# Kernel tuning notes

Hardware: AMD Instinct MI355X
Metric: run time of the kernel (lower is better)

Reference implementation:

```python
import math
import jax, jax.numpy as jnp
import numpy as np

HEADS = 8


def setup_inputs() -> dict:
    key = jax.random.key(0)
    k1, k2, k3 = jax.random.split(key, 3)
    b, n, a, dim = 1, 256, 256, 512
    init_scale = 0.02
    x = jax.random.normal(k1, (b, n, a, dim), dtype=jnp.float32)
    w_qkv = jax.random.normal(k2, (dim, 3 * dim), dtype=jnp.float32) * init_scale
    b_qkv = jnp.zeros((3 * dim,), dtype=jnp.float32)
    w_proj = jax.random.normal(k3, (dim, dim), dtype=jnp.float32) * init_scale
    b_proj = jnp.zeros((dim,), dtype=jnp.float32)
    return {"x": x, "w_qkv": w_qkv, "b_qkv": b_qkv, "w_proj": w_proj, "b_proj": b_proj}


def reference(x, w_qkv, b_qkv, w_proj, b_proj):
    b, n, a, dim = x.shape
    dh = dim // HEADS
    scale = 1.0 / math.sqrt(math.sqrt(dh))
    qkv = jnp.einsum('bnad,de->bnae', x, w_qkv) + b_qkv  # [b,n,a,3*dim]
    qkv = qkv.reshape(b, n, a, HEADS, 3 * dh)
    q, k, v = jnp.split(qkv, 3, axis=-1)  # each [b,n,a,h,dh]
    # scores over the 'a' axis, independent per (b, n, head)
    sim = jnp.einsum('bnihd,bnjhd->bnhij', q * scale, k * scale)
    attn = jax.nn.softmax(sim, axis=-1)
    out = jnp.einsum('bnhij,bnjhd->bnihd', attn, v).reshape(b, n, a, dim)
    return jnp.einsum('bnad,de->bnae', out, w_proj) + b_proj
```

## Files before the change

### kernel.cpp

```cpp
#include <hip/hip_runtime.h>

typedef unsigned short u16;
typedef unsigned int u32;
typedef __bf16 bf16x8 __attribute__((ext_vector_type(8)));
typedef float f32x4 __attribute__((ext_vector_type(4)));

__device__ __forceinline__ u16 f2b(float f) {
  u32 u = __builtin_bit_cast(u32, f);
  u32 r = (u + 0x7fffu + ((u >> 16) & 1u)) >> 16;
  return (u16)r;
}
__device__ __forceinline__ bf16x8 ld_frag(const u16* p) {
  uint4 v = *(const uint4*)p;
  return __builtin_bit_cast(bf16x8, v);
}
__device__ __forceinline__ void async_lds16(const u16* g, u16* lds) {
  __builtin_amdgcn_global_load_lds(
      (const __attribute__((address_space(1))) void*)g,
      (__attribute__((address_space(3))) void*)lds, 16, 0, 0);
}
__device__ __forceinline__ void wait_lds() { __builtin_amdgcn_s_waitcnt(0xc07f); }

__global__ __launch_bounds__(256) void convert_f32_bf16(const float* __restrict__ in,
                                                        u16* __restrict__ out) {
  long i = ((long)blockIdx.x * 256 + threadIdx.x) * 8;
  float4 a = *(const float4*)(in + i);
  float4 b = *(const float4*)(in + i + 4);
  union { uint4 v; u16 e[8]; } u;
  u.e[0] = f2b(a.x); u.e[1] = f2b(a.y); u.e[2] = f2b(a.z); u.e[3] = f2b(a.w);
  u.e[4] = f2b(b.x); u.e[5] = f2b(b.y); u.e[6] = f2b(b.z); u.e[7] = f2b(b.w);
  *(uint4*)(out + i) = u.v;
}

__global__ __launch_bounds__(256) void transpose_w(const float* __restrict__ W,
                                                   u16* __restrict__ Wt,
                                                   int K, int N) {
  __shared__ alignas(16) u16 T[64][80];
  const int n0 = blockIdx.x * 64, k0 = blockIdx.y * 64;
  const int t = threadIdx.x;
  {
    int kk = t >> 3, c = t & 7;
#pragma unroll
    for (int rr = 0; rr < 2; ++rr) {
      int kr = kk + rr * 32;
      const float* src = W + (long)(k0 + kr) * N + n0 + c * 8;
      float4 a = *(const float4*)src;
      float4 b = *(const float4*)(src + 4);
      u16* dst = &T[kr][c * 8];
      dst[0] = f2b(a.x); dst[1] = f2b(a.y); dst[2] = f2b(a.z); dst[3] = f2b(a.w);
      dst[4] = f2b(b.x); dst[5] = f2b(b.y); dst[6] = f2b(b.z); dst[7] = f2b(b.w);
    }
  }
  __syncthreads();
  {
    int nn = t >> 3, kc = t & 7;
#pragma unroll
    for (int rr = 0; rr < 2; ++rr) {
      int nr = nn + rr * 32;
      union { uint4 v; u16 e[8]; } u;
#pragma unroll
      for (int i = 0; i < 8; ++i) u.e[i] = T[kc * 8 + i][nr];
      *(uint4*)(Wt + (long)(n0 + nr) * K + k0 + kc * 8) = u.v;
    }
  }
}

template <bool OUT_F32>
__global__ __launch_bounds__(256) void gemm_bt(const u16* __restrict__ A,
                                               const u16* __restrict__ Bt,
                                               const float* __restrict__ bias,
                                               void* __restrict__ Cv,
                                               int M, int N, int K) {
  __shared__ alignas(16) u16 As[128 * 32];
  __shared__ alignas(16) u16 Bs[128 * 32];
  const int tid = threadIdx.x;
  const int lane = tid & 63, wave = tid >> 6;
  const int quad = lane >> 4, ln = lane & 15;
  const int wm = wave & 1, wn = wave >> 1;
  const long m0 = (long)blockIdx.y * 128;
  const long n0 = (long)blockIdx.x * 128;

  f32x4 zero = {0.f, 0.f, 0.f, 0.f};
  f32x4 acc[4][4];
#pragma unroll
  for (int i = 0; i < 4; ++i)
#pragma unroll
    for (int j = 0; j < 4; ++j) acc[i][j] = zero;

  const int c1 = tid + 256;
  const int rowA0 = tid >> 2, colA0 = (tid & 3) * 8;
  const int rowA1 = c1 >> 2, colA1 = (c1 & 3) * 8;
  u16* ldsA0 = &As[wave * 512];
  u16* ldsA1 = &As[2048 + wave * 512];
  u16* ldsB0 = &Bs[wave * 512];
  u16* ldsB1 = &Bs[2048 + wave * 512];

  for (int k0 = 0; k0 < K; k0 += 32) {
    async_lds16(A + (m0 + rowA0) * K + k0 + colA0, ldsA0);
    async_lds16(A + (m0 + rowA1) * K + k0 + colA1, ldsA1);
    async_lds16(Bt + (n0 + rowA0) * K + k0 + colA0, ldsB0);
    async_lds16(Bt + (n0 + rowA1) * K + k0 + colA1, ldsB1);
    __builtin_amdgcn_s_waitcnt(0x0f70);
    __syncthreads();
    bf16x8 af[4], bfr[4];
#pragma unroll
    for (int mt = 0; mt < 4; ++mt)
      af[mt] = ld_frag(&As[(wm * 64 + mt * 16 + ln) * 32 + quad * 8]);
#pragma unroll
    for (int nt = 0; nt < 4; ++nt)
      bfr[nt] = ld_frag(&Bs[(wn * 64 + nt * 16 + ln) * 32 + quad * 8]);
#pragma unroll
    for (int mt = 0; mt < 4; ++mt)
#pragma unroll
      for (int nt = 0; nt < 4; ++nt)
        acc[mt][nt] = __builtin_amdgcn_mfma_f32_16x16x32_bf16(af[mt], bfr[nt], acc[mt][nt], 0, 0, 0);
    __syncthreads();
  }

  if (OUT_F32) {
#pragma unroll
    for (int nt = 0; nt < 4; ++nt) {
      long coln = n0 + wn * 64 + nt * 16 + ln;
      float bv = bias[coln];
#pragma unroll
      for (int mt = 0; mt < 4; ++mt) {
        long rowb = m0 + wm * 64 + mt * 16 + quad * 4;
#pragma unroll
        for (int r = 0; r < 4; ++r)
          ((float*)Cv)[(rowb + r) * N + coln] = acc[mt][nt][r] + bv;
      }
    }
  } else {
    u16* buf = (wm == 0) ? As : Bs;
    for (int mt = 0; mt < 4; ++mt) {
      __syncthreads();
#pragma unroll
      for (int nt = 0; nt < 4; ++nt) {
        long coln = n0 + wn * 64 + nt * 16 + ln;
        float bv = bias[coln];
#pragma unroll
        for (int r = 0; r < 4; ++r)
          buf[(quad * 4 + r) * 136 + wn * 64 + nt * 16 + ln] = f2b(acc[mt][nt][r] + bv);
      }
      __syncthreads();
#pragma unroll
      for (int it = 0; it < 2; ++it) {
        int cid = it * 256 + tid;
        int bufi = cid >> 8, row = (cid >> 4) & 15, ch = cid & 15;
        const u16* sb = bufi ? Bs : As;
        uint4 v = *(const uint4*)&sb[row * 136 + ch * 8];
        *(uint4*)&((u16*)Cv)[(m0 + (long)bufi * 64 + mt * 16 + row) * N + n0 + ch * 8] = v;
      }
    }
  }
}

__global__ __launch_bounds__(256, 2) void attn_fused(const u16* __restrict__ qkv,
                                                     u16* __restrict__ out) {
  __shared__ alignas(16) u16 Ks[256 * 64];
  __shared__ alignas(16) u16 Vt[64 * 256];
  const int h = blockIdx.x;
  const long n = blockIdx.y;
  const int tid = threadIdx.x;
  const int lane = tid & 63, wave = tid >> 6;
  const int quad = lane >> 4, ln = lane & 15;
  const u16* base = qkv + (n * 256) * 1536 + h * 192;

  auto stageK = [&]() {
    int c = tid & 7, jb = tid >> 3;
#pragma unroll
    for (int rr = 0; rr < 8; ++rr) {
      int j = jb + rr * 32;
      uint4 v = *(const uint4*)(base + (long)j * 1536 + 64 + c * 8);
      *(uint4*)&Ks[j * 64 + ((c ^ (j & 7)) * 8)] = v;
    }
  };
  stageK();
  {
    int p = tid & 7, jb = tid >> 3;
#pragma unroll
    for (int rr = 0; rr < 8; ++rr) {
      int j = jb + rr * 32;
      union { uint4 v; u16 e[8]; } u;
      u.v = *(const uint4*)(base + (long)j * 1536 + 128 + p * 8);
      int cj = j >> 3, jl = j & 7;
#pragma unroll
      for (int i = 0; i < 8; ++i) {
        int d = p * 8 + i;
        int key = (p ^ i) & 7;
        Vt[d * 256 + ((cj ^ key) * 8) + jl] = u.e[i];
      }
    }
  }
  __syncthreads();

  u16* Pw = &Ks[wave * 2176];
  f32x4 zero = {0.f, 0.f, 0.f, 0.f};

  for (int s = 0; s < 2; ++s) {
    const int row0 = wave * 64 + s * 32;
    bf16x8 qa[2][2];
#pragma unroll
    for (int mt = 0; mt < 2; ++mt)
#pragma unroll
      for (int kc = 0; kc < 2; ++kc)
        qa[mt][kc] = ld_frag(base + (long)(row0 + mt * 16 + ln) * 1536 + kc * 32 + quad * 8);

    f32x4 sacc[2][16];
#pragma unroll
    for (int mt = 0; mt < 2; ++mt)
#pragma unroll
      for (int jt = 0; jt < 16; ++jt) sacc[mt][jt] = zero;

#pragma unroll
    for (int jt = 0; jt < 16; ++jt) {
#pragma unroll
      for (int kc = 0; kc < 2; ++kc) {
        bf16x8 kb = ld_frag(&Ks[(jt * 16 + ln) * 64 + (((kc * 4 + quad) ^ (ln & 7)) * 8)]);
        sacc[0][jt] = __builtin_amdgcn_mfma_f32_16x16x32_bf16(qa[0][kc], kb, sacc[0][jt], 0, 0, 0);
        sacc[1][jt] = __builtin_amdgcn_mfma_f32_16x16x32_bf16(qa[1][kc], kb, sacc[1][jt], 0, 0, 0);
      }
    }
    __syncthreads();

#pragma unroll
    for (int mt = 0; mt < 2; ++mt) {
      float linv[4];
#pragma unroll
      for (int r = 0; r < 4; ++r) {
        float mx = -3.0e38f;
#pragma unroll
        for (int jt = 0; jt < 16; ++jt) mx = fmaxf(mx, sacc[mt][jt][r]);
        mx = fmaxf(mx, __shfl_xor(mx, 1));
        mx = fmaxf(mx, __shfl_xor(mx, 2));
        mx = fmaxf(mx, __shfl_xor(mx, 4));
        mx = fmaxf(mx, __shfl_xor(mx, 8));
        float l = 0.f;
#pragma unroll
        for (int jt = 0; jt < 16; ++jt) {
          float p = __expf((sacc[mt][jt][r] - mx) * 0.125f);
          sacc[mt][jt][r] = p;
          l += p;
        }
        l += __shfl_xor(l, 1);
        l += __shfl_xor(l, 2);
        l += __shfl_xor(l, 4);
        l += __shfl_xor(l, 8);
        linv[r] = 1.0f / l;
      }

      f32x4 oacc[4];
#pragma unroll
      for (int dt = 0; dt < 4; ++dt) oacc[dt] = zero;
#pragma unroll
      for (int jh = 0; jh < 2; ++jh) {
#pragma unroll
        for (int jl = 0; jl < 8; ++jl) {
          int jt = jh * 8 + jl;
#pragma unroll
          for (int r = 0; r < 4; ++r)
            Pw[(quad * 4 + r) * 136 + jl * 16 + ln] = f2b(sacc[mt][jt][r]);
        }
        wait_lds();
#pragma unroll
        for (int jcl = 0; jcl < 4; ++jcl) {
          bf16x8 pa = ld_frag(&Pw[ln * 136 + jcl * 32 + quad * 8]);
          int cjb = (jh * 4 + jcl) * 4 + quad;
#pragma unroll
          for (int dt = 0; dt < 4; ++dt) {
            int d = dt * 16 + ln;
            int key = ((d >> 3) ^ d) & 7;
            bf16x8 vb = ld_frag(&Vt[d * 256 + ((cjb ^ key) * 8)]);
            oacc[dt] = __builtin_amdgcn_mfma_f32_16x16x32_bf16(pa, vb, oacc[dt], 0, 0, 0);
          }
        }
      }
#pragma unroll
      for (int dt = 0; dt < 4; ++dt)
#pragma unroll
        for (int r = 0; r < 4; ++r)
          Pw[(quad * 4 + r) * 136 + dt * 16 + ln] = f2b(oacc[dt][r] * linv[r]);
      wait_lds();
#pragma unroll
      for (int it = 0; it < 2; ++it) {
        int cid = it * 64 + lane;
        int row = cid >> 3, ch = cid & 7;
        uint4 v = *(const uint4*)&Pw[row * 136 + ch * 8];
        *(uint4*)&out[(n * 256 + row0 + mt * 16 + row) * 512 + h * 64 + ch * 8] = v;
      }
    }
    __syncthreads();
    if (s == 0) {
      stageK();
      __syncthreads();
    }
  }
}

extern "C" void kernel_launch(void* const* d_in, const int* in_sizes, int n_in,
                              void* d_out, int out_size, void* d_ws, size_t ws_size,
                              hipStream_t stream) {
  const float* x      = (const float*)d_in[0];
  const float* w_qkv  = (const float*)d_in[1];
  const float* b_qkv  = (const float*)d_in[2];
  const float* w_proj = (const float*)d_in[3];
  const float* b_proj = (const float*)d_in[4];
  float* out = (float*)d_out;

  char* ws = (char*)d_ws;
  u16* xb   = (u16*)ws;
  u16* qkv  = (u16*)(ws + 67108864L);
  u16* attn = (u16*)(ws + 67108864L + 201326592L);
  u16* Wt1  = (u16*)(ws + 67108864L + 201326592L + 67108864L);
  u16* Wt2  = Wt1 + 1536 * 512;

  convert_f32_bf16<<<16384, 256, 0, stream>>>(x, xb);
  transpose_w<<<dim3(24, 8), 256, 0, stream>>>(w_qkv, Wt1, 512, 1536);
  transpose_w<<<dim3(8, 8), 256, 0, stream>>>(w_proj, Wt2, 512, 512);
  gemm_bt<false><<<dim3(12, 512), 256, 0, stream>>>(xb, Wt1, b_qkv, qkv, 65536, 1536, 512);
  attn_fused<<<dim3(8, 256), 256, 0, stream>>>(qkv, attn);
  gemm_bt<true><<<dim3(4, 512), 256, 0, stream>>>(attn, Wt2, b_proj, out, 65536, 512, 512);
}
```

Before: 563.2 us.

## Replace GEMM with triple-buffered async pipeline, swizzled LDS and larger tiles

Rewrites both projection GEMMs as a 512-thread kernel with 256x128 tiles and K-step 64. Global-to-LDS loads are issued asynchronously into a three-stage ring buffer, with issue split across two halves of the MFMA loop. The kernel also adds an XOR swizzle on LDS rows to avoid bank conflicts, s_setprio around the MFMA blocks, and a grid remapping that groups blocks by XCD. The epilogue now uses per-wave LDS patches with no block barriers. This aims to hide memory latency and cut synchronisation overhead, at the cost of more LDS (144KB) and more complex wait-count bookkeeping.

```diff
diff --git a/kernel.cpp b/kernel.cpp
--- a/kernel.cpp
+++ b/kernel.cpp
@@ -66,19 +66,48 @@
 }
 
 template <bool OUT_F32>
-__global__ __launch_bounds__(256) void gemm_bt(const u16* __restrict__ A,
-                                               const u16* __restrict__ Bt,
-                                               const float* __restrict__ bias,
-                                               void* __restrict__ Cv,
-                                               int M, int N, int K) {
-  __shared__ alignas(16) u16 As[128 * 32];
-  __shared__ alignas(16) u16 Bs[128 * 32];
+__global__ __launch_bounds__(512, 2) void gemm_pipe(const u16* __restrict__ A,
+                                                    const u16* __restrict__ Bt,
+                                                    const float* __restrict__ bias,
+                                                    void* __restrict__ Cv,
+                                                    int M, int N, int K) {
+  __shared__ alignas(16) u16 lds[3 * 24576];
   const int tid = threadIdx.x;
   const int lane = tid & 63, wave = tid >> 6;
   const int quad = lane >> 4, ln = lane & 15;
-  const int wm = wave & 1, wn = wave >> 1;
-  const long m0 = (long)blockIdx.y * 128;
-  const long n0 = (long)blockIdx.x * 128;
+  const int wm = wave >> 1, wn = wave & 1;
+
+  const int nwg = gridDim.x;
+  const int bid = blockIdx.x;
+  const int wg = (bid & 7) * (nwg >> 3) + (bid >> 3);
+  const int ntn = N >> 7;
+  const int tn = wg % ntn, tm = wg / ntn;
+  const long m0 = (long)tm * 256;
+  const long n0 = (long)tn * 128;
+
+  const int rbase = wave * 8 + (lane >> 3);
+  const int swzch = ((lane & 7) ^ ((lane >> 3) & 7)) * 8;
+  const u16* gA[4];
+  const u16* gB[2];
+#pragma unroll
+  for (int u = 0; u < 4; ++u) gA[u] = A + (long)(m0 + u * 64 + rbase) * K + swzch;
+#pragma unroll
+  for (int u = 0; u < 2; ++u) gB[u] = Bt + (long)(n0 + u * 64 + rbase) * K + swzch;
+
+  auto stageA3 = [&](int t) {
+    long kst = (long)t * 64;
+    u16* sl = &lds[(t % 3) * 24576 + wave * 512];
+    async_lds16(gA[0] + kst, sl);
+    async_lds16(gA[1] + kst, sl + 4096);
+    async_lds16(gA[2] + kst, sl + 8192);
+  };
+  auto stageRest = [&](int t) {
+    long kst = (long)t * 64;
+    u16* sl = &lds[(t % 3) * 24576 + wave * 512];
+    async_lds16(gA[3] + kst, sl + 12288);
+    async_lds16(gB[0] + kst, sl + 16384);
+    async_lds16(gB[1] + kst, sl + 16384 + 4096);
+  };
 
   f32x4 zero = {0.f, 0.f, 0.f, 0.f};
   f32x4 acc[4][4];
@@ -87,35 +116,68 @@
 #pragma unroll
     for (int j = 0; j < 4; ++j) acc[i][j] = zero;
 
-  const int c1 = tid + 256;
-  const int rowA0 = tid >> 2, colA0 = (tid & 3) * 8;
-  const int rowA1 = c1 >> 2, colA1 = (c1 & 3) * 8;
-  u16* ldsA0 = &As[wave * 512];
-  u16* ldsA1 = &As[2048 + wave * 512];
-  u16* ldsB0 = &Bs[wave * 512];
-  u16* ldsB1 = &Bs[2048 + wave * 512];
-
-  for (int k0 = 0; k0 < K; k0 += 32) {
-    async_lds16(A + (m0 + rowA0) * K + k0 + colA0, ldsA0);
-    async_lds16(A + (m0 + rowA1) * K + k0 + colA1, ldsA1);
-    async_lds16(Bt + (n0 + rowA0) * K + k0 + colA0, ldsB0);
-    async_lds16(Bt + (n0 + rowA1) * K + k0 + colA1, ldsB1);
-    __builtin_amdgcn_s_waitcnt(0x0f70);
-    __syncthreads();
-    bf16x8 af[4], bfr[4];
-#pragma unroll
-    for (int mt = 0; mt < 4; ++mt)
-      af[mt] = ld_frag(&As[(wm * 64 + mt * 16 + ln) * 32 + quad * 8]);
+  const int KT = K >> 6;
+
+  stageA3(0); stageRest(0);
+  stageA3(1); stageRest(1);
+  __builtin_amdgcn_s_waitcnt(0x0f76);
+  __builtin_amdgcn_s_barrier();
+
+  for (int t = 0; t < KT; ++t) {
+    const u16* sl = &lds[(t % 3) * 24576];
+    bf16x8 bfr[4][2], af[2][2];
 #pragma unroll
     for (int nt = 0; nt < 4; ++nt)
-      bfr[nt] = ld_frag(&Bs[(wn * 64 + nt * 16 + ln) * 32 + quad * 8]);
-#pragma unroll
-    for (int mt = 0; mt < 4; ++mt)
+#pragma unroll
+      for (int ks = 0; ks < 2; ++ks) {
+        int row = wn * 64 + nt * 16 + ln;
+        bfr[nt][ks] = ld_frag(&sl[16384 + row * 64 + (((ks * 4 + quad) ^ (row & 7)) * 8)]);
+      }
+#pragma unroll
+    for (int mt = 0; mt < 2; ++mt)
+#pragma unroll
+      for (int ks = 0; ks < 2; ++ks) {
+        int row = wm * 64 + mt * 16 + ln;
+        af[mt][ks] = ld_frag(&sl[row * 64 + (((ks * 4 + quad) ^ (row & 7)) * 8)]);
+      }
+    if (t + 2 < KT) stageA3(t + 2);
+    __builtin_amdgcn_s_barrier();
+    __builtin_amdgcn_s_setprio(1);
+#pragma unroll
+    for (int mt = 0; mt < 2; ++mt)
 #pragma unroll
       for (int nt = 0; nt < 4; ++nt)
-        acc[mt][nt] = __builtin_amdgcn_mfma_f32_16x16x32_bf16(af[mt], bfr[nt], acc[mt][nt], 0, 0, 0);
-    __syncthreads();
-  }
+#pragma unroll
+        for (int ks = 0; ks < 2; ++ks)
+          acc[mt][nt] = __builtin_amdgcn_mfma_f32_16x16x32_bf16(af[mt][ks], bfr[nt][ks], acc[mt][nt], 0, 0, 0);
+    __builtin_amdgcn_s_setprio(0);
+    __builtin_amdgcn_s_barrier();
+#pragma unroll
+    for (int mt = 0; mt < 2; ++mt)
+#pragma unroll
+      for (int ks = 0; ks < 2; ++ks) {
+        int row = wm * 64 + (mt + 2) * 16 + ln;
+        af[mt][ks] = ld_frag(&sl[row * 64 + (((ks * 4 + quad) ^ (row & 7)) * 8)]);
+      }
+    if (t + 2 < KT) stageRest(t + 2);
+    __builtin_amdgcn_s_barrier();
+    __builtin_amdgcn_s_setprio(1);
+#pragma unroll
+    for (int mt = 0; mt < 2; ++mt)
+#pragma unroll
+      for (int nt = 0; nt < 4; ++nt)
+#pragma unroll
+        for (int ks = 0; ks < 2; ++ks)
+          acc[mt + 2][nt] = __builtin_amdgcn_mfma_f32_16x16x32_bf16(af[mt][ks], bfr[nt][ks], acc[mt + 2][nt], 0, 0, 0);
+    __builtin_amdgcn_s_setprio(0);
+    if (t + 1 < KT) {
+      if (t + 2 < KT) __builtin_amdgcn_s_waitcnt(0x0f76);
+      else            __builtin_amdgcn_s_waitcnt(0x0f70);
+    }
+    __builtin_amdgcn_s_barrier();
+  }
+
+  __syncthreads();
 
   if (OUT_F32) {
 #pragma unroll
@@ -131,26 +193,26 @@
       }
     }
   } else {
-    u16* buf = (wm == 0) ? As : Bs;
+    u16* patch = &lds[wave * 2176];
+    float bv[4];
+#pragma unroll
+    for (int nt = 0; nt < 4; ++nt) bv[nt] = bias[n0 + wn * 64 + nt * 16 + ln];
+#pragma unroll
     for (int mt = 0; mt < 4; ++mt) {
-      __syncthreads();
-#pragma unroll
-      for (int nt = 0; nt < 4; ++nt) {
-        long coln = n0 + wn * 64 + nt * 16 + ln;
-        float bv = bias[coln];
+#pragma unroll
+      for (int nt = 0; nt < 4; ++nt)
 #pragma unroll
         for (int r = 0; r < 4; ++r)
-          buf[(quad * 4 + r) * 136 + wn * 64 + nt * 16 + ln] = f2b(acc[mt][nt][r] + bv);
-      }
-      __syncthreads();
+          patch[(quad * 4 + r) * 136 + nt * 16 + ln] = f2b(acc[mt][nt][r] + bv[nt]);
+      wait_lds();
 #pragma unroll
       for (int it = 0; it < 2; ++it) {
-        int cid = it * 256 + tid;
-        int bufi = cid >> 8, row = (cid >> 4) & 15, ch = cid & 15;
-        const u16* sb = bufi ? Bs : As;
-        uint4 v = *(const uint4*)&sb[row * 136 + ch * 8];
-        *(uint4*)&((u16*)Cv)[(m0 + (long)bufi * 64 + mt * 16 + row) * N + n0 + ch * 8] = v;
-      }
+        int cid = it * 64 + lane;
+        int row = cid >> 3, ch = cid & 7;
+        uint4 v = *(const uint4*)&patch[row * 136 + ch * 8];
+        *(uint4*)&((u16*)Cv)[(m0 + wm * 64 + mt * 16 + row) * (long)N + n0 + wn * 64 + ch * 8] = v;
+      }
+      wait_lds();
     }
   }
 }
@@ -317,7 +379,7 @@
   convert_f32_bf16<<<16384, 256, 0, stream>>>(x, xb);
   transpose_w<<<dim3(24, 8), 256, 0, stream>>>(w_qkv, Wt1, 512, 1536);
   transpose_w<<<dim3(8, 8), 256, 0, stream>>>(w_proj, Wt2, 512, 512);
-  gemm_bt<false><<<dim3(12, 512), 256, 0, stream>>>(xb, Wt1, b_qkv, qkv, 65536, 1536, 512);
+  gemm_pipe<false><<<dim3(12 * 256), 512, 0, stream>>>(xb, Wt1, b_qkv, qkv, 65536, 1536, 512);
   attn_fused<<<dim3(8, 256), 256, 0, stream>>>(qkv, attn);
-  gemm_bt<true><<<dim3(4, 512), 256, 0, stream>>>(attn, Wt2, b_proj, out, 65536, 512, 512);
-}
+  gemm_pipe<true><<<dim3(4 * 256), 512, 0, stream>>>(attn, Wt2, b_proj, out, 65536, 512, 512);
+}
```

Result: no change. 570.2 us (+1.2%).

## Replace GEMM with triple-buffered async pipeline, swizzled LDS and larger tiles

Applied to the files above, without the earlier changes.

Rewrites the bf16 GEMM as a 512-thread kernel with 256x128 tiles, a three-stage async global-to-LDS pipeline with one barrier per k-step, an XOR-swizzled LDS layout and a grid remapping that interleaves workgroups across XCDs. MFMA sections get raised wave priority, and the bf16 epilogue writes through per-wave LDS patches without block-wide syncs. The aim is to overlap loads with MFMA work, cut bank conflicts and barriers, and improve L2 locality. It raises LDS use (72KB) and register pressure, which may limit occupancy.

```diff
diff --git a/kernel.cpp b/kernel.cpp
--- a/kernel.cpp
+++ b/kernel.cpp
@@ -66,19 +66,56 @@
 }
 
 template <bool OUT_F32>
-__global__ __launch_bounds__(256) void gemm_bt(const u16* __restrict__ A,
-                                               const u16* __restrict__ Bt,
-                                               const float* __restrict__ bias,
-                                               void* __restrict__ Cv,
-                                               int M, int N, int K) {
-  __shared__ alignas(16) u16 As[128 * 32];
-  __shared__ alignas(16) u16 Bs[128 * 32];
+__global__ __launch_bounds__(512, 4) void gemm_pipe(const u16* __restrict__ A,
+                                                    const u16* __restrict__ Bt,
+                                                    const float* __restrict__ bias,
+                                                    void* __restrict__ Cv,
+                                                    int M, int N, int K) {
+  __shared__ alignas(16) u16 lds[3 * 12288];
   const int tid = threadIdx.x;
   const int lane = tid & 63, wave = tid >> 6;
   const int quad = lane >> 4, ln = lane & 15;
-  const int wm = wave & 1, wn = wave >> 1;
-  const long m0 = (long)blockIdx.y * 128;
-  const long n0 = (long)blockIdx.x * 128;
+  const int wm = wave >> 1, wn = wave & 1;
+
+  const int nwg = gridDim.x;
+  const int bid = blockIdx.x;
+  const int wg = (bid & 7) * (nwg >> 3) + (bid >> 3);
+  const int ntn = N >> 7;
+  const int tn = wg % ntn, tm = wg / ntn;
+  const long m0 = (long)tm * 256;
+  const long n0 = (long)tn * 128;
+
+  const int R = tid >> 3, sp = tid & 7;
+  const int sl = sp ^ (R & 7);
+  const int sru = (R << 1) | (sl & 1);
+  const int scol = (sl >> 1) * 8;
+  const u16* gA0 = A + (m0 + sru) * (long)K + scol;
+  const u16* gA1 = A + (m0 + 128 + sru) * (long)K + scol;
+  const u16* gB0 = Bt + (n0 + sru) * (long)K + scol;
+
+  const int KT = K >> 5;
+
+  auto stage = [&](int t) {
+    if (t >= KT) return;
+    long ko = (long)t * 32;
+    u16* s = &lds[(t % 3) * 12288 + wave * 512];
+    async_lds16(gA0 + ko, s);
+    async_lds16(gA1 + ko, s + 4096);
+    async_lds16(gB0 + ko, s + 8192);
+  };
+
+  auto ldA = [&](int t, int mt) {
+    int ra = wm * 64 + mt * 16 + ln;
+    int u = ra >> 7, ru = ra & 127, Rr = ru >> 1;
+    int s2 = ((quad << 1) | (ru & 1)) ^ (Rr & 7);
+    return ld_frag(&lds[(t % 3) * 12288 + u * 4096 + Rr * 64 + s2 * 8]);
+  };
+  auto ldB = [&](int t, int nt) {
+    int rb = wn * 64 + nt * 16 + ln;
+    int Rr = rb >> 1;
+    int s2 = ((quad << 1) | (rb & 1)) ^ (Rr & 7);
+    return ld_frag(&lds[(t % 3) * 12288 + 8192 + Rr * 64 + s2 * 8]);
+  };
 
   f32x4 zero = {0.f, 0.f, 0.f, 0.f};
   f32x4 acc[4][4];
@@ -87,35 +124,29 @@
 #pragma unroll
     for (int j = 0; j < 4; ++j) acc[i][j] = zero;
 
-  const int c1 = tid + 256;
-  const int rowA0 = tid >> 2, colA0 = (tid & 3) * 8;
-  const int rowA1 = c1 >> 2, colA1 = (c1 & 3) * 8;
-  u16* ldsA0 = &As[wave * 512];
-  u16* ldsA1 = &As[2048 + wave * 512];
-  u16* ldsB0 = &Bs[wave * 512];
-  u16* ldsB1 = &Bs[2048 + wave * 512];
-
-  for (int k0 = 0; k0 < K; k0 += 32) {
-    async_lds16(A + (m0 + rowA0) * K + k0 + colA0, ldsA0);
-    async_lds16(A + (m0 + rowA1) * K + k0 + colA1, ldsA1);
-    async_lds16(Bt + (n0 + rowA0) * K + k0 + colA0, ldsB0);
-    async_lds16(Bt + (n0 + rowA1) * K + k0 + colA1, ldsB1);
-    __builtin_amdgcn_s_waitcnt(0x0f70);
-    __syncthreads();
-    bf16x8 af[4], bfr[4];
+  stage(0); stage(1);
+
+  for (int t = 0; t < KT; ++t) {
+    if (t < KT - 1) __builtin_amdgcn_s_waitcnt(0x0f73);
+    else            __builtin_amdgcn_s_waitcnt(0x0f70);
+    __builtin_amdgcn_s_barrier();
+    stage(t + 2);
+    bf16x8 a[4], b[4];
+#pragma unroll
+    for (int mt = 0; mt < 4; ++mt) a[mt] = ldA(t, mt);
+#pragma unroll
+    for (int nt = 0; nt < 4; ++nt) b[nt] = ldB(t, nt);
+    wait_lds();
+    __builtin_amdgcn_s_setprio(1);
 #pragma unroll
     for (int mt = 0; mt < 4; ++mt)
-      af[mt] = ld_frag(&As[(wm * 64 + mt * 16 + ln) * 32 + quad * 8]);
-#pragma unroll
-    for (int nt = 0; nt < 4; ++nt)
-      bfr[nt] = ld_frag(&Bs[(wn * 64 + nt * 16 + ln) * 32 + quad * 8]);
-#pragma unroll
-    for (int mt = 0; mt < 4; ++mt)
 #pragma unroll
       for (int nt = 0; nt < 4; ++nt)
-        acc[mt][nt] = __builtin_amdgcn_mfma_f32_16x16x32_bf16(af[mt], bfr[nt], acc[mt][nt], 0, 0, 0);
-    __syncthreads();
-  }
+        acc[mt][nt] = __builtin_amdgcn_mfma_f32_16x16x32_bf16(a[mt], b[nt], acc[mt][nt], 0, 0, 0);
+    __builtin_amdgcn_s_setprio(0);
+  }
+
+  __syncthreads();
 
   if (OUT_F32) {
 #pragma unroll
@@ -131,26 +162,26 @@
       }
     }
   } else {
-    u16* buf = (wm == 0) ? As : Bs;
+    u16* patch = &lds[wave * 2176];
+    float bv[4];
+#pragma unroll
+    for (int nt = 0; nt < 4; ++nt) bv[nt] = bias[n0 + wn * 64 + nt * 16 + ln];
+#pragma unroll
     for (int mt = 0; mt < 4; ++mt) {
-      __syncthreads();
-#pragma unroll
-      for (int nt = 0; nt < 4; ++nt) {
-        long coln = n0 + wn * 64 + nt * 16 + ln;
-        float bv = bias[coln];
+#pragma unroll
+      for (int nt = 0; nt < 4; ++nt)
 #pragma unroll
         for (int r = 0; r < 4; ++r)
-          buf[(quad * 4 + r) * 136 + wn * 64 + nt * 16 + ln] = f2b(acc[mt][nt][r] + bv);
-      }
-      __syncthreads();
+          patch[(quad * 4 + r) * 136 + nt * 16 + ln] = f2b(acc[mt][nt][r] + bv[nt]);
+      wait_lds();
 #pragma unroll
       for (int it = 0; it < 2; ++it) {
-        int cid = it * 256 + tid;
-        int bufi = cid >> 8, row = (cid >> 4) & 15, ch = cid & 15;
-        const u16* sb = bufi ? Bs : As;
-        uint4 v = *(const uint4*)&sb[row * 136 + ch * 8];
-        *(uint4*)&((u16*)Cv)[(m0 + (long)bufi * 64 + mt * 16 + row) * N + n0 + ch * 8] = v;
-      }
+        int cid = it * 64 + lane;
+        int row = cid >> 3, ch = cid & 7;
+        uint4 v = *(const uint4*)&patch[row * 136 + ch * 8];
+        *(uint4*)&((u16*)Cv)[(m0 + wm * 64 + mt * 16 + row) * (long)N + n0 + wn * 64 + ch * 8] = v;
+      }
+      wait_lds();
     }
   }
 }
@@ -317,7 +348,7 @@
   convert_f32_bf16<<<16384, 256, 0, stream>>>(x, xb);
   transpose_w<<<dim3(24, 8), 256, 0, stream>>>(w_qkv, Wt1, 512, 1536);
   transpose_w<<<dim3(8, 8), 256, 0, stream>>>(w_proj, Wt2, 512, 512);
-  gemm_bt<false><<<dim3(12, 512), 256, 0, stream>>>(xb, Wt1, b_qkv, qkv, 65536, 1536, 512);
+  gemm_pipe<false><<<dim3(3072), 512, 0, stream>>>(xb, Wt1, b_qkv, qkv, 65536, 1536, 512);
   attn_fused<<<dim3(8, 256), 256, 0, stream>>>(qkv, attn);
-  gemm_bt<true><<<dim3(4, 512), 256, 0, stream>>>(attn, Wt2, b_proj, out, 65536, 512, 512);
-}
+  gemm_pipe<true><<<dim3(1024), 512, 0, stream>>>(attn, Wt2, b_proj, out, 65536, 512, 512);
+}
```

After: 543.1 us. 3.6% less time.
